# Kernel optimization log

Measured on AMD Instinct MI355X. Metric: run time of the kernel, lower is better.

## Reference

```python
import jax, jax.numpy as jnp
import numpy as np

HIDDEN_DIM = 64
MEMORY_SLOTS = 8
SEQ_LEN = 64
VOCAB_SIZE = 64
B = 524288


def setup_inputs() -> dict:
    key = jax.random.key(0)
    k1, k2, k3, k4, k5, k6 = jax.random.split(key, 6)
    seqs = jax.random.randint(k1, (B, SEQ_LEN), 0, VOCAB_SIZE + 2, dtype=jnp.int64 if jax.config.jax_enable_x64 else jnp.int32)
    query_tok = jax.random.randint(k2, (B,), 0, VOCAB_SIZE + 2, dtype=seqs.dtype)
    embed = jax.random.normal(k3, (VOCAB_SIZE + 2, HIDDEN_DIM), dtype=jnp.float32)
    # torch Linear: y = x @ W.T + b
    W1 = jax.random.normal(k4, (HIDDEN_DIM, HIDDEN_DIM * 2), dtype=jnp.float32) * (1.0 / np.sqrt(HIDDEN_DIM * 2))
    b1 = jnp.zeros((HIDDEN_DIM,), dtype=jnp.float32)
    W2 = jax.random.normal(k5, (VOCAB_SIZE, HIDDEN_DIM), dtype=jnp.float32) * (1.0 / np.sqrt(HIDDEN_DIM))
    b2 = jnp.zeros((VOCAB_SIZE,), dtype=jnp.float32)
    return {"seqs": seqs, "query_tok": query_tok, "embed": embed,
            "W1": W1, "b1": b1, "W2": W2, "b2": b2}


def reference(seqs, query_tok, embed, W1, b1, W2, b2):
    # FIFO of capacity MEMORY_SLOTS over tokens t=0..SEQ_LEN-2 keeps exactly the
    # last MEMORY_SLOTS tokens: positions [SEQ_LEN-1-MEMORY_SLOTS, SEQ_LEN-1).
    win = seqs[:, SEQ_LEN - 1 - MEMORY_SLOTS : SEQ_LEN - 1]        # [B, 8]
    mem_summary = embed[win].mean(axis=1)                          # [B, H]
    q_emb = embed[query_tok]                                       # [B, H]
    h = jnp.concatenate([q_emb, mem_summary], axis=-1)             # [B, 2H]
    h = jax.nn.relu(h @ W1.T + b1)                                 # [B, H]
    logits = h @ W2.T + b2                                         # [B, VOCAB]
    return logits
```

## Files before the change

kernel.cpp:

```cpp
#include <hip/hip_runtime.h>

#define HID 64
#define NTOK 66
#define SEQ 64
#define WIN0 55
#define NW 8
#define LDS_STRIDE 72
#define ITERS 8
#define BLOCK 512
#define ROWS_PER_ITER 128
#define HOFF (2 * NTOK * LDS_STRIDE)
#define HSZ  (16 * LDS_STRIDE)

typedef _Float16 half8 __attribute__((ext_vector_type(8)));
typedef unsigned short ushort8v __attribute__((ext_vector_type(8)));
typedef float float4v __attribute__((ext_vector_type(4)));

static __device__ __forceinline__ unsigned short f2h(float f) {
    _Float16 h = (_Float16)f;
    union { _Float16 h; unsigned short u; } v; v.h = h;
    return v.u;
}

__global__ void build_tables(const float* __restrict__ embed,
                             const float* __restrict__ W1,
                             const float* __restrict__ b1,
                             unsigned short* __restrict__ tbl) {
    int b = blockIdx.x;
    int tb = b & 1;
    int t  = b >> 1;
    int n  = threadIdx.x;
    float acc = tb ? 0.0f : b1[n];
    const float* er = embed + t * HID;
    const float* wr = W1 + n * (2 * HID) + tb * HID;
#pragma unroll 8
    for (int k = 0; k < HID; ++k) acc += er[k] * wr[k];
    if (tb) acc *= 0.125f;
    tbl[tb * (NTOK * HID) + t * HID + n] = f2h(acc);
}

__global__ __launch_bounds__(BLOCK, 2) void fused_forward(
    const int* __restrict__ seqs,
    const int* __restrict__ qtok,
    const float* __restrict__ W2,
    const float* __restrict__ b2,
    const unsigned short* __restrict__ tbl,
    float* __restrict__ out)
{
    __shared__ unsigned short T_lds[HOFF + 8 * 2 * HSZ];

    int tid  = threadIdx.x;
    int wv   = tid >> 6;
    int l    = tid & 63;
    int lrow = l & 15;
    int lg   = l >> 4;
    int lk8  = lg * 8;
    int rgrp = l >> 3;
    int pchk = (l & 7) * 8;

    int blk0  = blockIdx.x * (ITERS * ROWS_PER_ITER);
    int crow0 = blk0 + wv * 16 + lrow;
    int prow0 = blk0 + wv * 16 + rgrp;

    unsigned short* hb = T_lds + HOFF + wv * (2 * HSZ);

    int qA0, qA1, qB0, qB1;
    int wA0[NW], wA1[NW], wB0[NW], wB1[NW];

#define LOADT(s, t_) { \
    int pr_ = prow0 + (t_) * ROWS_PER_ITER; \
    q##s##0 = qtok[pr_]; \
    q##s##1 = qtok[pr_ + 8]; \
    const int* s0_ = seqs + pr_ * SEQ + WIN0; \
    const int* s1_ = seqs + (pr_ + 8) * SEQ + WIN0; \
    _Pragma("unroll") \
    for (int j = 0; j < NW; ++j) { w##s##0[j] = s0_[j]; w##s##1[j] = s1_[j]; } \
}

#define RD_T1(qq) (*(const half8*)(T_lds + (qq) * LDS_STRIDE + pchk))
#define RD_T2(ww) (*(const half8*)(T_lds + NTOK * LDS_STRIDE + (ww) * LDS_STRIDE + pchk))

#define PRODUCE(s, buf_) { \
    half8 s0_ = RD_T1(q##s##0); \
    half8 s1_ = RD_T1(q##s##1); \
    _Pragma("unroll") \
    for (int j = 0; j < NW; ++j) { \
        s0_ += RD_T2(w##s##0[j]); \
        s1_ += RD_T2(w##s##1[j]); \
    } \
    half8 z_ = (half8)(_Float16)0; \
    s0_ = __builtin_elementwise_max(s0_, z_); \
    s1_ = __builtin_elementwise_max(s1_, z_); \
    *(half8*)(hb + (buf_) * HSZ + rgrp * LDS_STRIDE + pchk) = s0_; \
    *(half8*)(hb + (buf_) * HSZ + (rgrp + 8) * LDS_STRIDE + pchk) = s1_; \
}

#define CONSUME(t_, buf_) { \
    half8 a0 = *(const half8*)(hb + (buf_) * HSZ + lrow * LDS_STRIDE + lk8); \
    half8 a1 = *(const half8*)(hb + (buf_) * HSZ + lrow * LDS_STRIDE + 32 + lk8); \
    float* op = out + (size_t)(crow0 + (t_) * ROWS_PER_ITER) * HID; \
    _Pragma("unroll") \
    for (int nt = 0; nt < 4; ++nt) { \
        float4v acc_ = __builtin_amdgcn_mfma_f32_16x16x32_f16(wfrag[nt][0], a0, b2v[nt], 0, 0, 0); \
        acc_ = __builtin_amdgcn_mfma_f32_16x16x32_f16(wfrag[nt][1], a1, acc_, 0, 0, 0); \
        *(float4v*)(op + nt * 16 + lg * 4) = acc_; \
    } \
}

    LOADT(A, 0);
    LOADT(B, 1);

    half8   wfrag[4][2];
    float4v b2v[4];
#pragma unroll
    for (int nt = 0; nt < 4; ++nt) {
        b2v[nt] = *(const float4v*)(b2 + nt * 16 + lg * 4);
#pragma unroll
        for (int kc = 0; kc < 2; ++kc) {
            const float* wp = W2 + (nt * 16 + lrow) * HID + kc * 32 + lk8;
            half8 f;
#pragma unroll
            for (int j = 0; j < 8; ++j) f[j] = (_Float16)wp[j];
            wfrag[nt][kc] = f;
        }
    }

    for (int i = tid; i < 2 * NTOK * (HID / 8); i += BLOCK) {
        int tbi = i / (NTOK * 8);
        int rem = i - tbi * (NTOK * 8);
        int t   = rem >> 3;
        int kq  = (rem & 7) << 3;
        *(ushort8v*)(T_lds + tbi * (NTOK * LDS_STRIDE) + t * LDS_STRIDE + kq) =
            *(const ushort8v*)(tbl + tbi * (NTOK * HID) + t * HID + kq);
    }
    __syncthreads();

    PRODUCE(A, 0);
    LOADT(A, 2);

    PRODUCE(B, 1); CONSUME(0, 0); LOADT(B, 3);
    PRODUCE(A, 0); CONSUME(1, 1); LOADT(A, 4);
    PRODUCE(B, 1); CONSUME(2, 0); LOADT(B, 5);
    PRODUCE(A, 0); CONSUME(3, 1); LOADT(A, 6);
    PRODUCE(B, 1); CONSUME(4, 0); LOADT(B, 7);
    PRODUCE(A, 0); CONSUME(5, 1);
    PRODUCE(B, 1); CONSUME(6, 0);
                   CONSUME(7, 1);

#undef LOADT
#undef RD_T1
#undef RD_T2
#undef PRODUCE
#undef CONSUME
}

extern "C" void kernel_launch(void* const* d_in, const int* in_sizes, int n_in,
                              void* d_out, int out_size, void* d_ws, size_t ws_size,
                              hipStream_t stream) {
    const int*   seqs  = (const int*)d_in[0];
    const int*   qtok  = (const int*)d_in[1];
    const float* embed = (const float*)d_in[2];
    const float* W1    = (const float*)d_in[3];
    const float* b1    = (const float*)d_in[4];
    const float* W2    = (const float*)d_in[5];
    const float* b2    = (const float*)d_in[6];
    float* out = (float*)d_out;
    unsigned short* tbl = (unsigned short*)d_ws;

    int B = in_sizes[0] / SEQ;

    build_tables<<<NTOK * 2, HID, 0, stream>>>(embed, W1, b1, tbl);

    int grid = B / (ITERS * ROWS_PER_ITER);
    fused_forward<<<grid, BLOCK, 0, stream>>>(seqs, qtok, W2, b2, tbl, out);
}
```

Measured before the change: 50.10 us.

## Split waves into producer and consumer roles with block-level double buffering

Waves 0-3 now only gather the table rows and build the ReLU hidden tiles, while waves 4-7 only run the MFMA output projection, handing tiles through a shared double-buffered LDS region with a __syncthreads per iteration. Each block also processes twice as many row iterations, which halves the grid and amortizes the per-block table load into LDS. This separates memory-gather work from matrix and store work to overlap them, at the cost of block-wide barriers and idle lanes whenever the two roles are unbalanced.

```diff
diff --git a/kernel.cpp b/kernel.cpp
--- a/kernel.cpp
+++ b/kernel.cpp
@@ -6,11 +6,11 @@
 #define WIN0 55
 #define NW 8
 #define LDS_STRIDE 72
-#define ITERS 8
+#define ITERS 16
 #define BLOCK 512
 #define ROWS_PER_ITER 128
 #define HOFF (2 * NTOK * LDS_STRIDE)
-#define HSZ  (16 * LDS_STRIDE)
+#define HBUF (ROWS_PER_ITER * LDS_STRIDE)
 
 typedef _Float16 half8 __attribute__((ext_vector_type(8)));
 typedef unsigned short ushort8v __attribute__((ext_vector_type(8)));
@@ -47,7 +47,7 @@
     const unsigned short* __restrict__ tbl,
     float* __restrict__ out)
 {
-    __shared__ unsigned short T_lds[HOFF + 8 * 2 * HSZ];
+    __shared__ unsigned short T_lds[HOFF + 2 * HBUF];
 
     int tid  = threadIdx.x;
     int wv   = tid >> 6;
@@ -55,73 +55,100 @@
     int lrow = l & 15;
     int lg   = l >> 4;
     int lk8  = lg * 8;
-    int rgrp = l >> 3;
-    int pchk = (l & 7) * 8;
-
-    int blk0  = blockIdx.x * (ITERS * ROWS_PER_ITER);
-    int crow0 = blk0 + wv * 16 + lrow;
-    int prow0 = blk0 + wv * 16 + rgrp;
-
-    unsigned short* hb = T_lds + HOFF + wv * (2 * HSZ);
+    int tile0 = wv & 3;
+
+    int blk0 = blockIdx.x * (ITERS * ROWS_PER_ITER);
+    int prow0 = blk0 + tile0 * 16 + lrow;
+    int prow1 = prow0 + 64;
 
     int qA0, qA1, qB0, qB1;
     int wA0[NW], wA1[NW], wB0[NW], wB1[NW];
 
-#define LOADT(s, t_) { \
-    int pr_ = prow0 + (t_) * ROWS_PER_ITER; \
-    q##s##0 = qtok[pr_]; \
-    q##s##1 = qtok[pr_ + 8]; \
-    const int* s0_ = seqs + pr_ * SEQ + WIN0; \
-    const int* s1_ = seqs + (pr_ + 8) * SEQ + WIN0; \
+#define LOADT(S, t_) if ((t_) < ITERS) { \
+    int r0_ = prow0 + (t_) * ROWS_PER_ITER; \
+    int r1_ = prow1 + (t_) * ROWS_PER_ITER; \
+    q##S##0 = qtok[r0_]; \
+    q##S##1 = qtok[r1_]; \
+    const int* s0_ = seqs + r0_ * SEQ + WIN0; \
+    const int* s1_ = seqs + r1_ * SEQ + WIN0; \
     _Pragma("unroll") \
-    for (int j = 0; j < NW; ++j) { w##s##0[j] = s0_[j]; w##s##1[j] = s1_[j]; } \
-}
-
-#define RD_T1(qq) (*(const half8*)(T_lds + (qq) * LDS_STRIDE + pchk))
-#define RD_T2(ww) (*(const half8*)(T_lds + NTOK * LDS_STRIDE + (ww) * LDS_STRIDE + pchk))
-
-#define PRODUCE(s, buf_) { \
-    half8 s0_ = RD_T1(q##s##0); \
-    half8 s1_ = RD_T1(q##s##1); \
+    for (int j = 0; j < NW; ++j) { w##S##0[j] = s0_[j]; w##S##1[j] = s1_[j]; } \
+}
+
+#define RD_T1(qq, koff) (*(const half8*)(T_lds + (qq) * LDS_STRIDE + (koff)))
+#define RD_T2(ww, koff) (*(const half8*)(T_lds + NTOK * LDS_STRIDE + (ww) * LDS_STRIDE + (koff)))
+
+#define PRODUCE(S, buf_) { \
+    unsigned short* hb_ = T_lds + HOFF + (buf_) * HBUF; \
+    half8 s0_ = RD_T1(q##S##0, lk8); \
+    half8 s1_ = RD_T1(q##S##0, 32 + lk8); \
+    half8 u0_ = RD_T1(q##S##1, lk8); \
+    half8 u1_ = RD_T1(q##S##1, 32 + lk8); \
     _Pragma("unroll") \
     for (int j = 0; j < NW; ++j) { \
-        s0_ += RD_T2(w##s##0[j]); \
-        s1_ += RD_T2(w##s##1[j]); \
+        s0_ += RD_T2(w##S##0[j], lk8); \
+        s1_ += RD_T2(w##S##0[j], 32 + lk8); \
+        u0_ += RD_T2(w##S##1[j], lk8); \
+        u1_ += RD_T2(w##S##1[j], 32 + lk8); \
     } \
     half8 z_ = (half8)(_Float16)0; \
     s0_ = __builtin_elementwise_max(s0_, z_); \
     s1_ = __builtin_elementwise_max(s1_, z_); \
-    *(half8*)(hb + (buf_) * HSZ + rgrp * LDS_STRIDE + pchk) = s0_; \
-    *(half8*)(hb + (buf_) * HSZ + (rgrp + 8) * LDS_STRIDE + pchk) = s1_; \
+    u0_ = __builtin_elementwise_max(u0_, z_); \
+    u1_ = __builtin_elementwise_max(u1_, z_); \
+    unsigned short* r0_ = hb_ + (tile0 * 16 + lrow) * LDS_STRIDE; \
+    unsigned short* r1_ = hb_ + ((tile0 + 4) * 16 + lrow) * LDS_STRIDE; \
+    *(half8*)(r0_ + lk8) = s0_; \
+    *(half8*)(r0_ + 32 + lk8) = s1_; \
+    *(half8*)(r1_ + lk8) = u0_; \
+    *(half8*)(r1_ + 32 + lk8) = u1_; \
 }
 
 #define CONSUME(t_, buf_) { \
-    half8 a0 = *(const half8*)(hb + (buf_) * HSZ + lrow * LDS_STRIDE + lk8); \
-    half8 a1 = *(const half8*)(hb + (buf_) * HSZ + lrow * LDS_STRIDE + 32 + lk8); \
-    float* op = out + (size_t)(crow0 + (t_) * ROWS_PER_ITER) * HID; \
+    const unsigned short* hb_ = T_lds + HOFF + (buf_) * HBUF; \
     _Pragma("unroll") \
-    for (int nt = 0; nt < 4; ++nt) { \
-        float4v acc_ = __builtin_amdgcn_mfma_f32_16x16x32_f16(wfrag[nt][0], a0, b2v[nt], 0, 0, 0); \
-        acc_ = __builtin_amdgcn_mfma_f32_16x16x32_f16(wfrag[nt][1], a1, acc_, 0, 0, 0); \
-        *(float4v*)(op + nt * 16 + lg * 4) = acc_; \
+    for (int pt = 0; pt < 2; ++pt) { \
+        int trow_ = (tile0 + pt * 4) * 16 + lrow; \
+        half8 a0_ = *(const half8*)(hb_ + trow_ * LDS_STRIDE + lk8); \
+        half8 a1_ = *(const half8*)(hb_ + trow_ * LDS_STRIDE + 32 + lk8); \
+        float* op_ = out + (size_t)(blk0 + (t_) * ROWS_PER_ITER + trow_) * HID; \
+        _Pragma("unroll") \
+        for (int nt = 0; nt < 4; ++nt) { \
+            float4v acc_ = __builtin_amdgcn_mfma_f32_16x16x32_f16(wfrag[nt][0], a0_, b2v[nt], 0, 0, 0); \
+            acc_ = __builtin_amdgcn_mfma_f32_16x16x32_f16(wfrag[nt][1], a1_, acc_, 0, 0, 0); \
+            *(float4v*)(op_ + nt * 16 + lg * 4) = acc_; \
+        } \
     } \
 }
 
-    LOADT(A, 0);
-    LOADT(B, 1);
+#define ITER_E(t_) { \
+    if (wv >= 4) { CONSUME(t_, (t_) & 1); } \
+    else if ((t_) + 1 < ITERS) { PRODUCE(B, ((t_) + 1) & 1); LOADT(B, (t_) + 3); } \
+    __syncthreads(); \
+}
+#define ITER_O(t_) { \
+    if (wv >= 4) { CONSUME(t_, (t_) & 1); } \
+    else if ((t_) + 1 < ITERS) { PRODUCE(A, ((t_) + 1) & 1); LOADT(A, (t_) + 3); } \
+    __syncthreads(); \
+}
 
     half8   wfrag[4][2];
     float4v b2v[4];
+    if (wv < 4) {
+        LOADT(A, 0);
+        LOADT(B, 1);
+    } else {
 #pragma unroll
-    for (int nt = 0; nt < 4; ++nt) {
-        b2v[nt] = *(const float4v*)(b2 + nt * 16 + lg * 4);
+        for (int nt = 0; nt < 4; ++nt) {
+            b2v[nt] = *(const float4v*)(b2 + nt * 16 + lg * 4);
 #pragma unroll
-        for (int kc = 0; kc < 2; ++kc) {
-            const float* wp = W2 + (nt * 16 + lrow) * HID + kc * 32 + lk8;
-            half8 f;
+            for (int kc = 0; kc < 2; ++kc) {
+                const float* wp = W2 + (nt * 16 + lrow) * HID + kc * 32 + lk8;
+                half8 f;
 #pragma unroll
-            for (int j = 0; j < 8; ++j) f[j] = (_Float16)wp[j];
-            wfrag[nt][kc] = f;
+                for (int j = 0; j < 8; ++j) f[j] = (_Float16)wp[j];
+                wfrag[nt][kc] = f;
+            }
         }
     }
 
@@ -135,23 +162,24 @@
     }
     __syncthreads();
 
-    PRODUCE(A, 0);
-    LOADT(A, 2);
-
-    PRODUCE(B, 1); CONSUME(0, 0); LOADT(B, 3);
-    PRODUCE(A, 0); CONSUME(1, 1); LOADT(A, 4);
-    PRODUCE(B, 1); CONSUME(2, 0); LOADT(B, 5);
-    PRODUCE(A, 0); CONSUME(3, 1); LOADT(A, 6);
-    PRODUCE(B, 1); CONSUME(4, 0); LOADT(B, 7);
-    PRODUCE(A, 0); CONSUME(5, 1);
-    PRODUCE(B, 1); CONSUME(6, 0);
-                   CONSUME(7, 1);
+    if (wv < 4) {
+        PRODUCE(A, 0);
+        LOADT(A, 2);
+    }
+    __syncthreads();
+
+    ITER_E(0);  ITER_O(1);  ITER_E(2);  ITER_O(3);
+    ITER_E(4);  ITER_O(5);  ITER_E(6);  ITER_O(7);
+    ITER_E(8);  ITER_O(9);  ITER_E(10); ITER_O(11);
+    ITER_E(12); ITER_O(13); ITER_E(14); ITER_O(15);
 
 #undef LOADT
 #undef RD_T1
 #undef RD_T2
 #undef PRODUCE
 #undef CONSUME
+#undef ITER_E
+#undef ITER_O
 }
 
 extern "C" void kernel_launch(void* const* d_in, const int* in_sizes, int n_in,
```

Measured after the change: 44.80 us. 10.6% less time.
